# Optimization experiments

Hardware: AMD Instinct MI355X
Metric: run time of the kernel (lower is better)

Reference implementation:

```python
import jax, jax.numpy as jnp
import numpy as np
import math

D_MODEL = 1024
NUM_HEADS = 16
SEQ = 2048
BATCH = 4


def setup_inputs() -> dict:
    key = jax.random.key(0)
    ks = jax.random.split(key, 7)
    s = 0.02
    return {
        "x": jax.random.normal(ks[0], (BATCH, SEQ, D_MODEL), jnp.float32),
        "Wq": jax.random.normal(ks[1], (D_MODEL, D_MODEL), jnp.float32) * s,
        "bq": jax.random.normal(ks[2], (D_MODEL,), jnp.float32) * s,
        "Wkv": jax.random.normal(ks[3], (D_MODEL, 2 * D_MODEL), jnp.float32) * s,
        "bkv": jax.random.normal(ks[4], (2 * D_MODEL,), jnp.float32) * s,
        "Wo": jax.random.normal(ks[5], (D_MODEL, D_MODEL), jnp.float32) * s,
        "bo": jax.random.normal(ks[6], (D_MODEL,), jnp.float32) * s,
        "decoderMask": 1,
    }


def reference(x, Wq, bq, Wkv, bkv, Wo, bo, decoderMask):
    B, S, D = x.shape
    H = NUM_HEADS
    dh = D // H
    q_ = x @ Wq + bq              # [B,S,D]
    kv_ = x @ Wkv + bkv           # [B,S,2D] (self-attention: m is None)
    # Faithful to source: concat [q_, kv_] then reshape into heads of 3*dh,
    # which interleaves Q/KV projection columns across heads.
    qkv = jnp.concatenate([q_, kv_], axis=-1)          # [B,S,3D]
    qkv = qkv.reshape(B, S, H, 3 * dh).transpose(0, 2, 1, 3)  # [B,H,S,3dh]
    q, k, v = jnp.split(qkv, 3, axis=-1)               # each [B,H,S,dh]
    scaled = jnp.einsum("bhqd,bhkd->bhqk", q, k) / math.sqrt(dh)
    if decoderMask:
        mask = jnp.triu(jnp.full((S, S), -jnp.inf, dtype=scaled.dtype), k=1)
        scaled = scaled + mask
    attn = jax.nn.softmax(scaled, axis=-1)
    vals = jnp.einsum("bhqk,bhkd->bhqd", attn, v)      # [B,H,S,dh]
    vals = vals.transpose(0, 2, 1, 3).reshape(B, S, D)
    return vals @ Wo + bo
```

## Files before the change

kernel.cpp:

```cpp
#include <hip/hip_runtime.h>
#include <cstddef>
#include <cstdint>

#define SEQ   2048
#define BATCH 4
#define DM    1024
#define NH    16
#define DH    64
#define ROWS  (BATCH*SEQ)
#define NC3   3072
#define SM_SCALE 0.18033688f

typedef unsigned short u16;
typedef __attribute__((ext_vector_type(8))) short bf16x8;
typedef __attribute__((ext_vector_type(2))) float f32x2;
typedef __attribute__((ext_vector_type(4))) float f32x4;
typedef __attribute__((ext_vector_type(16))) float f32x16;
typedef __attribute__((ext_vector_type(4))) unsigned u32x4;
typedef __attribute__((ext_vector_type(2))) unsigned u32x2;

union V16 { f32x16 v; f32x2 p[8]; };

__device__ __forceinline__ u16 f2b(float f) {
  union { float f; unsigned u; } v; v.f = f;
  unsigned r = v.u + 0x7fffu + ((v.u >> 16) & 1u);
  return (u16)(r >> 16);
}

__device__ __forceinline__ unsigned cvt_pk_bf16(float lo, float hi) {
  unsigned r;
  asm("v_cvt_pk_bf16_f32 %0, %1, %2" : "=v"(r) : "v"(lo), "v"(hi));
  return r;
}

__device__ __forceinline__ void plswap(unsigned& a, unsigned& b) {
  auto rr = __builtin_amdgcn_permlane32_swap((int)a, (int)b, false, false);
  a = (unsigned)rr[0];
  b = (unsigned)rr[1];
}

__device__ __forceinline__ float ex2(float x) { return __builtin_amdgcn_exp2f(x); }

__device__ __forceinline__ void gld16(const void* g, void* l) {
  __builtin_amdgcn_global_load_lds((const __attribute__((address_space(1))) void*)g,
                                   (__attribute__((address_space(3))) void*)l,
                                   16, 0, 0);
}

__global__ __launch_bounds__(256) void prep_tw_kernel(
    const float* __restrict__ x, const float* __restrict__ bq,
    const float* __restrict__ bkv, u16* __restrict__ xb, float* __restrict__ bc,
    const float* __restrict__ Wq, const float* __restrict__ Wkv,
    const float* __restrict__ Wo, u16* __restrict__ Wt)
{
  __shared__ float t_[32][33];
  const int tid = threadIdx.x;
  if (blockIdx.x < 8192) {
    int i = blockIdx.x * 256 + tid;
    int idx = i * 4;
    float4 v = *(const float4*)(x + idx);
    u32x2 pv;
    pv[0] = cvt_pk_bf16(v.x, v.y);
    pv[1] = cvt_pk_bf16(v.z, v.w);
    *(u32x2*)&xb[idx] = pv;
    if (i < NC3) bc[i] = (i < DM) ? bq[i] : bkv[i - DM];
  } else {
    const int bid = blockIdx.x - 8192;
    const int n0 = (bid & 127) * 32, k0 = (bid >> 7) * 32;
    const int xcol = tid & 31, yrow = tid >> 5;
    #pragma unroll
    for (int it = 0; it < 4; ++it) {
      int k = k0 + yrow + it * 8;
      int n = n0 + xcol;
      float v;
      if (n < DM)           v = Wq[k * DM + n];
      else if (n < NC3)     v = Wkv[k * (2 * DM) + (n - DM)];
      else                  v = Wo[k * DM + (n - NC3)];
      t_[yrow + it * 8][xcol] = v;
    }
    __syncthreads();
    #pragma unroll
    for (int it = 0; it < 4; ++it) {
      int n = n0 + yrow + it * 8;
      int k = k0 + xcol;
      Wt[(size_t)n * DM + k] = f2b(t_[xcol][yrow + it * 8]);
    }
  }
}

__global__ __launch_bounds__(512, 2) void gemm8_qkv(
    const u16* __restrict__ A, const u16* __restrict__ Bt,
    const float* __restrict__ bias, u16* __restrict__ C, u16* __restrict__ Vt)
{
  constexpr int K = 1024, N = NC3;
  constexpr int ASLOT = 16384;
  constexpr int BBASE = 32768;
  constexpr int BSLOT = 12288;
  __shared__ alignas(16) u16 lds_[57344];

  const int tid = threadIdx.x;
  const int lane = tid & 63, wid = tid >> 6;
  const int wr2 = wid >> 2, wc4 = wid & 3;
  const int l15 = lane & 15, lhi = lane >> 4;

  const int bid = blockIdx.x;
  const int xcd = bid & 7, t = bid >> 3;
  const int row0 = (xcd * 4 + (t & 3)) * 256;
  const int hh   = t >> 2;
  const int col0 = hh * 192;

  const int sr = tid >> 3;
  const int scg = ((tid & 7) ^ (sr & 7)) * 8;
  const u16* aSrc = A  + (size_t)(row0 + sr) * K + scg;
  const u16* bSrc = Bt + (size_t)(col0 + sr) * K + scg;
  const int dLin = tid * 8;

  auto stA = [&](int kt, int u) {
    gld16(aSrc + (size_t)(u * 64) * K + kt * 64,
          lds_ + (kt & 1) * ASLOT + u * 4096 + dLin);
  };
  auto stB = [&](int kt, int u) {
    gld16(bSrc + (size_t)(u * 64) * K + kt * 64,
          lds_ + BBASE + (kt & 1) * BSLOT + u * 4096 + dLin);
  };

  int csw[2];
  csw[0] = ((lhi)     ^ (l15 & 7)) * 8;
  csw[1] = ((4 + lhi) ^ (l15 & 7)) * 8;
  const int aBase = wr2 * 8192 + l15 * 64;
  const int bBase = BBASE + (wc4 * 48 + l15) * 64;

  f32x4 acc[8][3];
  #pragma unroll
  for (int m = 0; m < 8; ++m)
    #pragma unroll
    for (int n = 0; n < 3; ++n) { f32x4 z = {0.f, 0.f, 0.f, 0.f}; acc[m][n] = z; }

  stA(0, 0); stA(0, 1); stA(0, 2); stA(0, 3);
  stB(0, 0); stB(0, 1); stB(0, 2);
  stB(1, 0); stB(1, 1); stB(1, 2);
  asm volatile("s_waitcnt vmcnt(3)" ::: "memory");
  __builtin_amdgcn_s_barrier();

  constexpr int KT2 = K / 128;
  for (int j = 0; j < KT2; ++j) {
    const bool last = (j == KT2 - 1);
    #pragma unroll
    for (int hk = 0; hk < 2; ++hk) {
      const int slotA = hk * ASLOT;
      const int slotB = hk * BSLOT;
      bf16x8 bfr[3][2];
      #pragma unroll
      for (int ph = 0; ph < 4; ++ph) {
        const int gp = hk * 4 + ph;
        if (ph == 0) {
          #pragma unroll
          for (int n = 0; n < 3; ++n)
            #pragma unroll
            for (int kk = 0; kk < 2; ++kk)
              bfr[n][kk] = *(const bf16x8*)&lds_[bBase + slotB + n * 1024 + csw[kk]];
        }
        bf16x8 af[2][2];
        #pragma unroll
        for (int mi = 0; mi < 2; ++mi)
          #pragma unroll
          for (int kk = 0; kk < 2; ++kk)
            af[mi][kk] = *(const bf16x8*)&lds_[aBase + slotA + (ph * 2 + mi) * 1024 + csw[kk]];
        switch (gp) {
          case 0: stA(2 * j + 1, 0); stA(2 * j + 1, 1); break;
          case 1: stA(2 * j + 1, 2); stA(2 * j + 1, 3); break;
          case 2: if (!last) { stB(2 * j + 2, 0); stB(2 * j + 2, 1); } break;
          case 3: if (!last) { stB(2 * j + 2, 2); } break;
          case 4: if (!last) { stA(2 * j + 2, 0); stA(2 * j + 2, 1); } break;
          case 5: if (!last) { stA(2 * j + 2, 2); stA(2 * j + 2, 3); } break;
          case 6: if (!last) { stB(2 * j + 3, 0); stB(2 * j + 3, 1); } break;
          case 7: if (!last) { stB(2 * j + 3, 2); } break;
        }
        __builtin_amdgcn_s_barrier();
        asm volatile("s_waitcnt lgkmcnt(0)" ::: "memory");
        __builtin_amdgcn_sched_barrier(0);
        __builtin_amdgcn_s_setprio(1);
        #pragma unroll
        for (int mi = 0; mi < 2; ++mi)
          #pragma unroll
          for (int n = 0; n < 3; ++n) {
            acc[ph * 2 + mi][n] =
                __builtin_amdgcn_mfma_f32_16x16x32_bf16(af[mi][0], bfr[n][0], acc[ph * 2 + mi][n], 0, 0, 0);
            acc[ph * 2 + mi][n] =
                __builtin_amdgcn_mfma_f32_16x16x32_bf16(af[mi][1], bfr[n][1], acc[ph * 2 + mi][n], 0, 0, 0);
          }
        __builtin_amdgcn_s_setprio(0);
        if (gp == 3) {
          if (last) { asm volatile("s_waitcnt vmcnt(0)" ::: "memory"); }
          else      { asm volatile("s_waitcnt vmcnt(3)" ::: "memory"); }
        } else if (gp == 7 && !last) {
          asm volatile("s_waitcnt vmcnt(3)" ::: "memory");
        }
        __builtin_amdgcn_s_barrier();
      }
    }
  }

  #pragma unroll
  for (int m = 0; m < 8; ++m) {
    const int row = row0 + wr2 * 128 + m * 16 + lhi * 4;
    #pragma unroll
    for (int n = 0; n < 3; ++n) {
      const int cc  = wc4 * 48 + n * 16 + l15;
      const int col = col0 + cc;
      const float bv = bias[col];
      if (cc < 128) {
        const float qs = (cc < 64) ? SM_SCALE : 1.f;
        #pragma unroll
        for (int r = 0; r < 4; ++r)
          C[(size_t)(row + r) * N + col] = f2b((acc[m][n][r] + bv) * qs);
      } else {
        u16 wv[4];
        #pragma unroll
        for (int r = 0; r < 4; ++r) wv[r] = f2b(acc[m][n][r] + bv);
        const int bb = row >> 11, jj = row & (SEQ - 1);
        u16* vt = Vt + ((size_t)(bb * NH + hh) * 64 + (cc - 128)) * SEQ + jj;
        u32x2 pv = { (unsigned)wv[0] | ((unsigned)wv[1] << 16),
                     (unsigned)wv[2] | ((unsigned)wv[3] << 16) };
        *(u32x2*)vt = pv;
      }
    }
  }
}

__global__ __launch_bounds__(512, 2) void gemm8_out(
    const u16* __restrict__ A, const u16* __restrict__ Bt,
    const float* __restrict__ bias, float* __restrict__ C)
{
  constexpr int K = 1024, N = DM;
  constexpr int ASLOT = 16384;
  constexpr int BBASE = 32768;
  constexpr int BSLOT = 8192;
  __shared__ alignas(16) u16 lds_[49152];

  const int tid = threadIdx.x;
  const int lane = tid & 63, wid = tid >> 6;
  const int wr2 = wid >> 2, wc4 = wid & 3;
  const int l15 = lane & 15, lhi = lane >> 4;

  const int bid = blockIdx.x;
  const int xcd = bid & 7, t = bid >> 3;
  const int row0 = (xcd * 4 + (t & 3)) * 256;
  const int col0 = (t >> 2) * 128;

  const int sr = tid >> 3;
  const int scg = ((tid & 7) ^ (sr & 7)) * 8;
  const u16* aSrc = A  + (size_t)(row0 + sr) * K + scg;
  const u16* bSrc = Bt + (size_t)(col0 + sr) * K + scg;
  const int dLin = tid * 8;

  auto stA = [&](int kt, int u) {
    gld16(aSrc + (size_t)(u * 64) * K + kt * 64,
          lds_ + (kt & 1) * ASLOT + u * 4096 + dLin);
  };
  auto stB = [&](int kt, int u) {
    gld16(bSrc + (size_t)(u * 64) * K + kt * 64,
          lds_ + BBASE + (kt & 1) * BSLOT + u * 4096 + dLin);
  };

  int csw[2];
  csw[0] = ((lhi)     ^ (l15 & 7)) * 8;
  csw[1] = ((4 + lhi) ^ (l15 & 7)) * 8;
  const int aBase = wr2 * 8192 + l15 * 64;
  const int bBase = BBASE + (wc4 * 32 + l15) * 64;

  f32x4 acc[8][2];
  #pragma unroll
  for (int m = 0; m < 8; ++m)
    #pragma unroll
    for (int n = 0; n < 2; ++n) { f32x4 z = {0.f, 0.f, 0.f, 0.f}; acc[m][n] = z; }

  stA(0, 0); stA(0, 1); stA(0, 2); stA(0, 3);
  stB(0, 0); stB(0, 1);
  stB(1, 0); stB(1, 1);
  asm volatile("s_waitcnt vmcnt(2)" ::: "memory");
  __builtin_amdgcn_s_barrier();

  constexpr int KT2 = K / 128;
  for (int j = 0; j < KT2; ++j) {
    const bool last = (j == KT2 - 1);
    #pragma unroll
    for (int hk = 0; hk < 2; ++hk) {
      const int slotA = hk * ASLOT;
      const int slotB = hk * BSLOT;
      bf16x8 bfr[2][2];
      #pragma unroll
      for (int ph = 0; ph < 4; ++ph) {
        const int gp = hk * 4 + ph;
        if (ph == 0) {
          #pragma unroll
          for (int n = 0; n < 2; ++n)
            #pragma unroll
            for (int kk = 0; kk < 2; ++kk)
              bfr[n][kk] = *(const bf16x8*)&lds_[bBase + slotB + n * 1024 + csw[kk]];
        }
        bf16x8 af[2][2];
        #pragma unroll
        for (int mi = 0; mi < 2; ++mi)
          #pragma unroll
          for (int kk = 0; kk < 2; ++kk)
            af[mi][kk] = *(const bf16x8*)&lds_[aBase + slotA + (ph * 2 + mi) * 1024 + csw[kk]];
        switch (gp) {
          case 0: stA(2 * j + 1, 0); stA(2 * j + 1, 1); break;
          case 1: stA(2 * j + 1, 2); stA(2 * j + 1, 3); break;
          case 2: if (!last) { stB(2 * j + 2, 0); stB(2 * j + 2, 1); } break;
          case 4: if (!last) { stA(2 * j + 2, 0); stA(2 * j + 2, 1); } break;
          case 5: if (!last) { stA(2 * j + 2, 2); stA(2 * j + 2, 3); } break;
          case 6: if (!last) { stB(2 * j + 3, 0); stB(2 * j + 3, 1); } break;
          default: break;
        }
        __builtin_amdgcn_s_barrier();
        asm volatile("s_waitcnt lgkmcnt(0)" ::: "memory");
        __builtin_amdgcn_sched_barrier(0);
        __builtin_amdgcn_s_setprio(1);
        #pragma unroll
        for (int mi = 0; mi < 2; ++mi)
          #pragma unroll
          for (int n = 0; n < 2; ++n) {
            acc[ph * 2 + mi][n] =
                __builtin_amdgcn_mfma_f32_16x16x32_bf16(af[mi][0], bfr[n][0], acc[ph * 2 + mi][n], 0, 0, 0);
            acc[ph * 2 + mi][n] =
                __builtin_amdgcn_mfma_f32_16x16x32_bf16(af[mi][1], bfr[n][1], acc[ph * 2 + mi][n], 0, 0, 0);
          }
        __builtin_amdgcn_s_setprio(0);
        if (gp == 3) {
          if (last) { asm volatile("s_waitcnt vmcnt(0)" ::: "memory"); }
          else      { asm volatile("s_waitcnt vmcnt(2)" ::: "memory"); }
        } else if (gp == 7 && !last) {
          asm volatile("s_waitcnt vmcnt(2)" ::: "memory");
        }
        __builtin_amdgcn_s_barrier();
      }
    }
  }

  #pragma unroll
  for (int m = 0; m < 8; ++m) {
    const int row = row0 + wr2 * 128 + m * 16 + lhi * 4;
    #pragma unroll
    for (int n = 0; n < 2; ++n) {
      const int col = col0 + wc4 * 32 + n * 16 + l15;
      const float bv = bias[col];
      #pragma unroll
      for (int r = 0; r < 4; ++r)
        C[(size_t)(row + r) * N + col] = acc[m][n][r] + bv;
    }
  }
}

__global__ __launch_bounds__(512, 2) void attn_kernel(
    const u16* __restrict__ qkv, const u16* __restrict__ Vt, u16* __restrict__ ctx)
{
  const int bid = blockIdx.x;
  const int p   = (bid >> 3) & 7;
  const int g   = (bid & 7) + ((bid >> 6) << 3);
  const int h   = g & 15, b = g >> 4;
  const int tid = threadIdx.x;
  const int lane = tid & 63;
  const int hf  = tid >> 8;
  const int wid2 = (tid >> 6) & 3;
  const int l31 = lane & 31, lhi5 = lane >> 5;

  __shared__ alignas(16) u16 smem[40960];
  u16* const AQ = smem;
  u16* const KV = smem + 8192 + hf * 16384;

  const int bTiles = 16 - 2 * p;
  const int qtA = 8 + p;
  const int qtSelf = hf ? (7 - p) : qtA;

  const size_t kv_row = (size_t)(b * NH + h) * 64;
  const int st = tid & 255;
  const int sr = st >> 3, sck = st & 7;
  const int scks = sck ^ (sr & 7);

  const u16* kSrc0 = qkv + (size_t)(b * SEQ + sr) * NC3 + h * 192 + 64 + scks * 8;
  const u16* kSrc1 = kSrc0 + (size_t)32 * NC3;
  const u16* vSrc0 = Vt + (kv_row + sr) * SEQ + scks * 8;
  const u16* vSrc1 = vSrc0 + (size_t)32 * SEQ;
  const int dOff0 = sr * 64 + sck * 8;
  const int dOff1 = (32 + sr) * 64 + sck * 8;

  auto stageKV = [&](int jt, u16* buf) {
    const size_t kAdv = (size_t)(jt * 64) * NC3;
    const int    vAdv = jt * 64;
    gld16(kSrc0 + kAdv, buf + dOff0);
    gld16(kSrc1 + kAdv, buf + dOff1);
    gld16(vSrc0 + vAdv, buf + 4096 + dOff0);
    gld16(vSrc1 + vAdv, buf + 4096 + dOff1);
  };

  int koff[4], koff2[4];
  #pragma unroll
  for (int c = 0; c < 4; ++c) {
    koff[c]  = l31 * 64        + (((2 * c + lhi5) ^ (l31 & 7)) * 8);
    koff2[c] = (32 + l31) * 64 + (((2 * c + lhi5) ^ (l31 & 7)) * 8);
  }

  {
    const int q0S = qtSelf * 128;
    u16* const QDST = hf ? KV : AQ;
    #pragma unroll
    for (int it = 0; it < 4; ++it) {
      int row = it * 32 + sr;
      gld16(qkv + (size_t)(b * SEQ + q0S + row) * NC3 + h * 192 + scks * 8,
            QDST + row * 64 + sck * 8);
    }
    stageKV(0, KV + 8192);
  }
  __syncthreads();

  bf16x8 qf[4];
  {
    const int qrow = wid2 * 32 + l31;
    const u16* qsrc = hf ? KV : AQ;
    #pragma unroll
    for (int c = 0; c < 4; ++c)
      qf[c] = *(const bf16x8*)&qsrc[qrow * 64 + (((2 * c + lhi5) ^ (qrow & 7)) * 8)];
  }
  __syncthreads();

  V16 o0, o1;
  #pragma unroll
  for (int r = 0; r < 16; ++r) { o0.v[r] = 0.f; o1.v[r] = 0.f; }
  float lrow = 0.f;

  int q0  = qtSelf * 128;
  int qw0 = q0 + wid2 * 32;
  int qa  = qw0 + l31;
  int dqb = qa - 4 * lhi5;

  auto storeOut = [&]() {
    const float inv = 1.f / lrow;
    u16* crow = ctx + (size_t)(b * SEQ + qa) * DM + h * DH;
    #pragma unroll
    for (int i = 0; i < 4; ++i) {
      u32x2 v0, v1;
      v0[0] = cvt_pk_bf16(o0.v[4 * i + 0] * inv, o0.v[4 * i + 1] * inv);
      v0[1] = cvt_pk_bf16(o0.v[4 * i + 2] * inv, o0.v[4 * i + 3] * inv);
      v1[0] = cvt_pk_bf16(o1.v[4 * i + 0] * inv, o1.v[4 * i + 1] * inv);
      v1[1] = cvt_pk_bf16(o1.v[4 * i + 2] * inv, o1.v[4 * i + 3] * inv);
      *(u32x2*)&crow[8 * i + 4 * lhi5]      = v0;
      *(u32x2*)&crow[32 + 8 * i + 4 * lhi5] = v1;
    }
  };

  #pragma unroll 1
  for (int it = 0; it < 17; ++it) {
    if (hf == 1 && it == bTiles) {
      storeOut();
      #pragma unroll
      for (int r = 0; r < 16; ++r) { o0.v[r] = 0.f; o1.v[r] = 0.f; }
      lrow = 0.f;
      q0 = qtA * 128; qw0 = q0 + wid2 * 32; qa = qw0 + l31; dqb = qa - 4 * lhi5;
      const int qrow = wid2 * 32 + l31;
      #pragma unroll
      for (int c = 0; c < 4; ++c)
        qf[c] = *(const bf16x8*)&AQ[qrow * 64 + (((2 * c + lhi5) ^ (qrow & 7)) * 8)];
    }

    const int jt = (hf == 0) ? it : (it < bTiles ? it : 17 + (it - bTiles));
    const int j0 = jt * 64;
    const u16* buf = KV + ((it + 1) & 1) * 8192;
    const u16* Kb = buf;
    const u16* Vb = buf + 4096;

    if (it + 1 < 17) {
      const int itN = it + 1;
      const int jtN = (hf == 0) ? itN : (itN < bTiles ? itN : 17 + (itN - bTiles));
      stageKV(jtN, KV + (it & 1) * 8192);
    }

    if (j0 <= qw0 + 31) {
      V16 s0, s1;
      #pragma unroll
      for (int r = 0; r < 16; ++r) { s0.v[r] = 0.f; s1.v[r] = 0.f; }
      __builtin_amdgcn_s_setprio(1);
      #pragma unroll
      for (int c = 0; c < 4; ++c) {
        bf16x8 kf = *(const bf16x8*)&Kb[koff[c]];
        s0.v = __builtin_amdgcn_mfma_f32_32x32x16_bf16(kf, qf[c], s0.v, 0, 0, 0);
      }
      #pragma unroll
      for (int c = 0; c < 4; ++c) {
        bf16x8 kf = *(const bf16x8*)&Kb[koff2[c]];
        s1.v = __builtin_amdgcn_mfma_f32_32x32x16_bf16(kf, qf[c], s1.v, 0, 0, 0);
      }
      __builtin_amdgcn_s_setprio(0);

      if (j0 + 63 > qw0) {
        const int dq = dqb - j0;
        #pragma unroll
        for (int r = 0; r < 16; ++r) {
          const int kvc = (r & 3) + 8 * (r >> 2);
          s0.v[r] = (kvc > dq)      ? -1e30f : s0.v[r];
          s1.v[r] = (kvc + 32 > dq) ? -1e30f : s1.v[r];
        }
      }

      f32x2 sum2 = {0.f, 0.f};
      #pragma unroll
      for (int i = 0; i < 8; ++i) {
        f32x2 e0, e1;
        e0[0] = ex2(s0.p[i][0]); e0[1] = ex2(s0.p[i][1]);
        e1[0] = ex2(s1.p[i][0]); e1[1] = ex2(s1.p[i][1]);
        s0.p[i] = e0; s1.p[i] = e1;
        sum2 += e0 + e1;
      }
      float ps = sum2[0] + sum2[1];
      {
        unsigned a = __builtin_bit_cast(unsigned, ps), bb = a;
        plswap(a, bb);
        ps = __builtin_bit_cast(float, a) + __builtin_bit_cast(float, bb);
      }
      lrow += ps;

      unsigned pk0[8], pk1[8];
      #pragma unroll
      for (int i = 0; i < 4; ++i) {
        pk0[2 * i]     = cvt_pk_bf16(s0.v[4 * i + 0], s0.v[4 * i + 1]);
        pk0[2 * i + 1] = cvt_pk_bf16(s0.v[4 * i + 2], s0.v[4 * i + 3]);
        pk1[2 * i]     = cvt_pk_bf16(s1.v[4 * i + 0], s1.v[4 * i + 1]);
        pk1[2 * i + 1] = cvt_pk_bf16(s1.v[4 * i + 2], s1.v[4 * i + 3]);
      }
      bf16x8 pf[4];
      {
        unsigned a0 = pk0[0], b0 = pk0[2]; plswap(a0, b0);
        unsigned a1 = pk0[1], b1 = pk0[3]; plswap(a1, b1);
        u32x4 w0v = {a0, a1, b0, b1}; pf[0] = __builtin_bit_cast(bf16x8, w0v);
        unsigned a2 = pk0[4], b2 = pk0[6]; plswap(a2, b2);
        unsigned a3 = pk0[5], b3 = pk0[7]; plswap(a3, b3);
        u32x4 w1v = {a2, a3, b2, b3}; pf[1] = __builtin_bit_cast(bf16x8, w1v);
        unsigned a4 = pk1[0], b4 = pk1[2]; plswap(a4, b4);
        unsigned a5 = pk1[1], b5 = pk1[3]; plswap(a5, b5);
        u32x4 w2v = {a4, a5, b4, b5}; pf[2] = __builtin_bit_cast(bf16x8, w2v);
        unsigned a6 = pk1[4], b6 = pk1[6]; plswap(a6, b6);
        unsigned a7 = pk1[5], b7 = pk1[7]; plswap(a7, b7);
        u32x4 w3v = {a6, a7, b6, b7}; pf[3] = __builtin_bit_cast(bf16x8, w3v);
      }

      __builtin_amdgcn_s_setprio(1);
      #pragma unroll
      for (int c = 0; c < 4; ++c) {
        bf16x8 vf = *(const bf16x8*)&Vb[koff[c]];
        o0.v = __builtin_amdgcn_mfma_f32_32x32x16_bf16(vf, pf[c], o0.v, 0, 0, 0);
      }
      #pragma unroll
      for (int c = 0; c < 4; ++c) {
        bf16x8 vf = *(const bf16x8*)&Vb[koff2[c]];
        o1.v = __builtin_amdgcn_mfma_f32_32x32x16_bf16(vf, pf[c], o1.v, 0, 0, 0);
      }
      __builtin_amdgcn_s_setprio(0);
    }
    __syncthreads();
  }

  float* const poA = (float*)(smem + 8192);
  float* const plA = (float*)smem;
  if (hf == 1) {
    const int base2 = st * 32;
    #pragma unroll
    for (int i = 0; i < 16; ++i) { poA[base2 + i] = o0.v[i]; poA[base2 + 16 + i] = o1.v[i]; }
    plA[st] = lrow;
  }
  __syncthreads();
  if (hf == 0) {
    const int base2 = st * 32;
    #pragma unroll
    for (int i = 0; i < 16; ++i) { o0.v[i] += poA[base2 + i]; o1.v[i] += poA[base2 + 16 + i]; }
    lrow += plA[st];
    storeOut();
  }
}

extern "C" void kernel_launch(void* const* d_in, const int* in_sizes, int n_in,
                              void* d_out, int out_size, void* d_ws, size_t ws_size,
                              hipStream_t stream) {
  (void)in_sizes; (void)n_in; (void)out_size; (void)ws_size;
  const float* x   = (const float*)d_in[0];
  const float* Wq  = (const float*)d_in[1];
  const float* bq  = (const float*)d_in[2];
  const float* Wkv = (const float*)d_in[3];
  const float* bkv = (const float*)d_in[4];
  const float* Wo  = (const float*)d_in[5];
  const float* bo  = (const float*)d_in[6];
  float* out = (float*)d_out;

  char* w = (char*)d_ws;
  size_t off = 0;
  auto alloc = [&](size_t bytes) { void* p = w + off; off += (bytes + 255) & ~(size_t)255; return p; };
  u16*   xb   = (u16*)alloc((size_t)ROWS * DM * 2);
  u16*   qkvb = (u16*)alloc((size_t)ROWS * NC3 * 2);
  u16*   Vt   = (u16*)alloc((size_t)BATCH * NH * DH * SEQ * 2);
  u16*   Wt   = (u16*)alloc((size_t)4096 * DM * 2);
  float* bc   = (float*)alloc((size_t)NC3 * 4);
  u16*   ctx  = xb;

  prep_tw_kernel<<<dim3(8192 + 4096), 256, 0, stream>>>(x, bq, bkv, xb, bc, Wq, Wkv, Wo, Wt);
  gemm8_qkv<<<dim3(512), 512, 0, stream>>>(xb, Wt, bc, qkvb, Vt);
  attn_kernel<<<dim3(512), 512, 0, stream>>>(qkvb, Vt, ctx);
  gemm8_out<<<dim3(256), 512, 0, stream>>>(ctx, Wt + (size_t)NC3 * DM, bo, out);
}
```

Baseline: 149.6 us.

## Load V fragments directly from global memory instead of staging through LDS

V tiles are no longer staged into shared memory. Each wave reads its V MFMA fragments straight from global (Vt) memory inside the compute loop, and only K stays double-buffered in LDS. This shrinks LDS use from 80KB to 48KB and cuts LDS write/read traffic for V. The cost is that every wave redundantly issues uncoalesced-ish global loads for V, and their latency is exposed inside the loop rather than prefetched a tile ahead. An extra barrier is also added before the first K stage.

```diff
diff --git a/kernel.cpp b/kernel.cpp
--- a/kernel.cpp
+++ b/kernel.cpp
@@ -366,9 +366,9 @@
   const int wid2 = (tid >> 6) & 3;
   const int l31 = lane & 31, lhi5 = lane >> 5;
 
-  __shared__ alignas(16) u16 smem[40960];
+  __shared__ alignas(16) u16 smem[24576];
   u16* const AQ = smem;
-  u16* const KV = smem + 8192 + hf * 16384;
+  u16* const KB = smem + 8192 + hf * 8192;
 
   const int bTiles = 16 - 2 * p;
   const int qtA = 8 + p;
@@ -381,18 +381,16 @@
 
   const u16* kSrc0 = qkv + (size_t)(b * SEQ + sr) * NC3 + h * 192 + 64 + scks * 8;
   const u16* kSrc1 = kSrc0 + (size_t)32 * NC3;
-  const u16* vSrc0 = Vt + (kv_row + sr) * SEQ + scks * 8;
-  const u16* vSrc1 = vSrc0 + (size_t)32 * SEQ;
   const int dOff0 = sr * 64 + sck * 8;
   const int dOff1 = (32 + sr) * 64 + sck * 8;
 
-  auto stageKV = [&](int jt, u16* buf) {
+  const u16* vB0 = Vt + (kv_row + l31) * SEQ + lhi5 * 8;
+  const u16* vB1 = Vt + (kv_row + 32 + l31) * SEQ + lhi5 * 8;
+
+  auto stageK = [&](int jt, u16* buf) {
     const size_t kAdv = (size_t)(jt * 64) * NC3;
-    const int    vAdv = jt * 64;
     gld16(kSrc0 + kAdv, buf + dOff0);
     gld16(kSrc1 + kAdv, buf + dOff1);
-    gld16(vSrc0 + vAdv, buf + 4096 + dOff0);
-    gld16(vSrc1 + vAdv, buf + 4096 + dOff1);
   };
 
   int koff[4], koff2[4];
@@ -404,25 +402,27 @@
 
   {
     const int q0S = qtSelf * 128;
-    u16* const QDST = hf ? KV : AQ;
+    u16* const QDST = hf ? KB : AQ;
     #pragma unroll
     for (int it = 0; it < 4; ++it) {
       int row = it * 32 + sr;
       gld16(qkv + (size_t)(b * SEQ + q0S + row) * NC3 + h * 192 + scks * 8,
             QDST + row * 64 + sck * 8);
     }
-    stageKV(0, KV + 8192);
   }
   __syncthreads();
 
   bf16x8 qf[4];
   {
     const int qrow = wid2 * 32 + l31;
-    const u16* qsrc = hf ? KV : AQ;
+    const u16* qsrc = hf ? KB : AQ;
     #pragma unroll
     for (int c = 0; c < 4; ++c)
       qf[c] = *(const bf16x8*)&qsrc[qrow * 64 + (((2 * c + lhi5) ^ (qrow & 7)) * 8)];
   }
+  __syncthreads();
+
+  stageK(0, KB + 4096);
   __syncthreads();
 
   V16 o0, o1;
@@ -466,14 +466,12 @@
 
     const int jt = (hf == 0) ? it : (it < bTiles ? it : 17 + (it - bTiles));
     const int j0 = jt * 64;
-    const u16* buf = KV + ((it + 1) & 1) * 8192;
-    const u16* Kb = buf;
-    const u16* Vb = buf + 4096;
+    const u16* Kb = KB + ((it + 1) & 1) * 4096;
 
     if (it + 1 < 17) {
       const int itN = it + 1;
       const int jtN = (hf == 0) ? itN : (itN < bTiles ? itN : 17 + (itN - bTiles));
-      stageKV(jtN, KV + (it & 1) * 8192);
+      stageK(jtN, KB + (it & 1) * 4096);
     }
 
     if (j0 <= qw0 + 31) {
@@ -519,6 +517,13 @@
         ps = __builtin_bit_cast(float, a) + __builtin_bit_cast(float, bb);
       }
       lrow += ps;
+
+      bf16x8 vf0[4], vf1[4];
+      #pragma unroll
+      for (int c = 0; c < 4; ++c) {
+        vf0[c] = *(const bf16x8*)(vB0 + j0 + c * 16);
+        vf1[c] = *(const bf16x8*)(vB1 + j0 + c * 16);
+      }
 
       unsigned pk0[8], pk1[8];
       #pragma unroll
@@ -546,15 +551,11 @@
 
       __builtin_amdgcn_s_setprio(1);
       #pragma unroll
-      for (int c = 0; c < 4; ++c) {
-        bf16x8 vf = *(const bf16x8*)&Vb[koff[c]];
-        o0.v = __builtin_amdgcn_mfma_f32_32x32x16_bf16(vf, pf[c], o0.v, 0, 0, 0);
-      }
-      #pragma unroll
-      for (int c = 0; c < 4; ++c) {
-        bf16x8 vf = *(const bf16x8*)&Vb[koff2[c]];
-        o1.v = __builtin_amdgcn_mfma_f32_32x32x16_bf16(vf, pf[c], o1.v, 0, 0, 0);
-      }
+      for (int c = 0; c < 4; ++c)
+        o0.v = __builtin_amdgcn_mfma_f32_32x32x16_bf16(vf0[c], pf[c], o0.v, 0, 0, 0);
+      #pragma unroll
+      for (int c = 0; c < 4; ++c)
+        o1.v = __builtin_amdgcn_mfma_f32_32x32x16_bf16(vf1[c], pf[c], o1.v, 0, 0, 0);
       __builtin_amdgcn_s_setprio(0);
     }
     __syncthreads();
```

Result: slower. 195.8 us (+30.9%).
